# Optimization experiments

Measured on AMD Instinct MI355X. Metric: run time of the kernel, lower is better.

The kernel has to match this reference:

```python
import jax, jax.numpy as jnp
import numpy as np

B, S, D, H = 2, 2048, 1024, 16
DH = D // H

def setup_inputs() -> dict:
    key = jax.random.key(0)
    ks = jax.random.split(key, 11)
    sc = 0.02
    return {
        "q_": jax.random.normal(ks[0], (B, S, D), jnp.float32),
        "k_": jax.random.normal(ks[1], (B, S, D), jnp.float32),
        "v_": jax.random.normal(ks[2], (B, S, D), jnp.float32),
        "mask": jnp.ones((B, S), dtype=bool),
        "Wq": jax.random.normal(ks[3], (D, D), jnp.float32) * sc,
        "bq": jnp.zeros((D,), jnp.float32),
        "Wk": jax.random.normal(ks[4], (D, D), jnp.float32) * sc,
        "bk": jnp.zeros((D,), jnp.float32),
        "Wv": jax.random.normal(ks[5], (D, D), jnp.float32) * sc,
        "bv": jnp.zeros((D,), jnp.float32),
        "Wf": jax.random.normal(ks[6], (D, D), jnp.float32) * sc,
        "bf": jnp.zeros((D,), jnp.float32),
    }

def _split_heads(x, b):
    # [B, S, D] -> [B, H, S, DH]
    return x.reshape(b, -1, H, DH).transpose(0, 2, 1, 3)

def reference(q_, k_, v_, mask, Wq, bq, Wk, bk, Wv, bv, Wf, bf):
    b = q_.shape[0]
    q = _split_heads(q_ @ Wq + bq, b)
    k = _split_heads(k_ @ Wk + bk, b)
    v = _split_heads(v_ @ Wv + bv, b)
    # scaled dot-product attention scores [B, H, Sq, Sk]
    attn = jnp.einsum('bhqd,bhkd->bhqk', q, k) / jnp.sqrt(jnp.float32(DH))
    # original mask pattern: mask[B,S] repeated over heads then over KEY axis,
    # i.e. it masks whole query rows, broadcast over keys
    attn = jnp.where(mask[:, None, :, None], attn, jnp.float32(-1e12))
    attn_score = jax.nn.softmax(attn, axis=-1)  # dropout is identity (eval / drop=0)
    out = jnp.einsum('bhqk,bhkd->bhqd', attn_score, v)
    out = out.transpose(0, 2, 1, 3).reshape(b, -1, D)  # [B, S, D]
    return (out + q_) @ Wf + bf
```

## Files before the change

kernel.cpp:

```cpp
#include <hip/hip_runtime.h>
#include <stdint.h>


typedef __attribute__((ext_vector_type(8))) short bf16x8;
typedef __attribute__((ext_vector_type(4))) float f32x4;

#define MFMA(a, b, c) __builtin_amdgcn_mfma_f32_16x16x32_bf16((a), (b), (c), 0, 0, 0)

__device__ __forceinline__ short f2b(float f) {
  unsigned u = __builtin_bit_cast(unsigned, f);
  unsigned r = (u + 0x7fffu + ((u >> 16) & 1u)) >> 16;
  return (short)r;
}
__device__ __forceinline__ float b2f(short s) {
  unsigned u = ((unsigned)(unsigned short)s) << 16;
  return __builtin_bit_cast(float, u);
}
__device__ __forceinline__ void gload16(const void* g, void* l) {
  __builtin_amdgcn_global_load_lds((const __attribute__((address_space(1))) void*)g,
                                   (__attribute__((address_space(3))) void*)l, 16, 0, 0);
}

__global__ __launch_bounds__(256) void prep(const float* __restrict__ q,
                                            const float* __restrict__ k,
                                            const float* __restrict__ v,
                                            short* __restrict__ qb,
                                            short* __restrict__ kb,
                                            short* __restrict__ vb,
                                            const float* __restrict__ W0, const float* __restrict__ W1,
                                            const float* __restrict__ W2, const float* __restrict__ W3,
                                            short* __restrict__ T0, short* __restrict__ T1,
                                            short* __restrict__ T2, short* __restrict__ T3) {
  __shared__ float t[32][33];
  const int z = blockIdx.z;
  if (z < 3) {
    const float* src = (z == 0) ? q : (z == 1) ? k : v;
    short* dst       = (z == 0) ? qb : (z == 1) ? kb : vb;
    const int i = (blockIdx.x * 256 + threadIdx.x) * 8;
    const float4 f0 = *(const float4*)(src + i);
    const float4 f1 = *(const float4*)(src + i + 4);
    unsigned ou[4];
    ou[0] = (unsigned short)f2b(f0.x) | ((unsigned)(unsigned short)f2b(f0.y) << 16);
    ou[1] = (unsigned short)f2b(f0.z) | ((unsigned)(unsigned short)f2b(f0.w) << 16);
    ou[2] = (unsigned short)f2b(f1.x) | ((unsigned)(unsigned short)f2b(f1.y) << 16);
    ou[3] = (unsigned short)f2b(f1.z) | ((unsigned)(unsigned short)f2b(f1.w) << 16);
    *(uint4*)(dst + i) = *(uint4*)ou;
  } else {
    const int c = threadIdx.x & 31, r0 = threadIdx.x >> 5;
#pragma unroll
    for (int rep = 0; rep < 2; ++rep) {
      const int tile = blockIdx.x + rep * 2048;
      const int mtx = tile >> 10;
      const float* W = (mtx == 0) ? W0 : (mtx == 1) ? W1 : (mtx == 2) ? W2 : W3;
      short* T       = (mtx == 0) ? T0 : (mtx == 1) ? T1 : (mtx == 2) ? T2 : T3;
      const int n0 = (tile & 31) << 5, k0 = ((tile >> 5) & 31) << 5;
      if (rep) __syncthreads();
#pragma unroll
      for (int p = 0; p < 4; ++p) {
        int r = r0 + p * 8;
        t[r][c] = W[(size_t)(k0 + r) * 1024 + n0 + c];
      }
      __syncthreads();
#pragma unroll
      for (int p = 0; p < 4; ++p) {
        int r = r0 + p * 8;
        T[(size_t)(n0 + r) * 1024 + k0 + c] = f2b(t[c][r]);
      }
    }
  }
}

template <int MODE, int DBUF, int BM, int FVT>
__global__ __launch_bounds__(256) void gemm_bt(
    const short* __restrict__ A0, const short* __restrict__ A1, const short* __restrict__ A2_,
    const short* __restrict__ T0, const short* __restrict__ T1, const short* __restrict__ T2,
    const float* __restrict__ b0, const float* __restrict__ b1, const float* __restrict__ b2,
    void* o0, void* o1, void* o2) {
  constexpr int MT = BM / 32;
  __shared__ short As[(DBUF + 1) * BM * 64];
  __shared__ short Bs[(DBUF + 1) * 128 * 64];
  const int z = blockIdx.z;
  const short* A  = (z == 0) ? A0 : (z == 1) ? A1 : A2_;
  const short* Bt = (z == 0) ? T0 : (z == 1) ? T1 : T2;
  const float* bias = (z == 0) ? b0 : (z == 1) ? b1 : b2;
  void* outp = (z == 0) ? o0 : (z == 1) ? o1 : o2;
  const bool vt = (FVT == 2) || (FVT == 1 && z == 2);

  const int tid = threadIdx.x;
  const int lane = tid & 63, wid = tid >> 6;
  const int hi = lane >> 4, lo = lane & 15;
  const int wm = (wid >> 1) * (BM / 2), wn = (wid & 1) << 6;
  const int m0 = blockIdx.x * BM, n0 = blockIdx.y << 7;

  f32x4 acc[MT][4] = {};

  auto stage = [&](int bsel, int k0) {
    short* Ad = As + bsel * (BM * 64);
    short* Bd = Bs + bsel * 8192;
#pragma unroll
    for (int s = 0; s < BM / 32; ++s) {
      int d = s * 256 + tid;
      int row = d >> 3, cc = d & 7;
      int sc = cc ^ (row & 7);
      gload16(A + (size_t)(m0 + row) * 1024 + k0 + sc * 8, (void*)(Ad + (d & ~63) * 8));
    }
#pragma unroll
    for (int s = 0; s < 4; ++s) {
      int d = s * 256 + tid;
      int row = d >> 3, cc = d & 7;
      int sc = cc ^ (row & 7);
      gload16(Bt + (size_t)(n0 + row) * 1024 + k0 + sc * 8, (void*)(Bd + (d & ~63) * 8));
    }
  };
  auto compute = [&](const short* Asb, const short* Bsb) {
    bf16x8 af[MT][2], bfr[4][2];
#pragma unroll
    for (int t = 0; t < MT; ++t)
#pragma unroll
      for (int kh = 0; kh < 2; ++kh) {
        int ra = wm + t * 16 + lo;
        af[t][kh] = *(const bf16x8*)(Asb + ra * 64 + ((((kh << 2) | hi) ^ (ra & 7)) * 8));
      }
#pragma unroll
    for (int t = 0; t < 4; ++t)
#pragma unroll
      for (int kh = 0; kh < 2; ++kh) {
        int rb = wn + t * 16 + lo;
        bfr[t][kh] = *(const bf16x8*)(Bsb + rb * 64 + ((((kh << 2) | hi) ^ (rb & 7)) * 8));
      }
#pragma unroll
    for (int kh = 0; kh < 2; ++kh)
#pragma unroll
      for (int mt = 0; mt < MT; ++mt)
#pragma unroll
        for (int nt = 0; nt < 4; ++nt)
          acc[mt][nt] = MFMA(af[mt][kh], bfr[nt][kh], acc[mt][nt]);
  };

  if (DBUF) {
    stage(0, 0);
#pragma unroll 2
    for (int t = 0; t < 16; ++t) {
      __syncthreads();
      if (t < 15) stage((t + 1) & 1, (t + 1) * 64);
      compute(As + (t & 1) * (BM * 64), Bs + (t & 1) * 8192);
    }
  } else {
    for (int k0 = 0; k0 < 1024; k0 += 64) {
      stage(0, k0);
      __syncthreads();
      compute(As, Bs);
      __syncthreads();
    }
  }

#pragma unroll
  for (int mt = 0; mt < MT; ++mt) {
#pragma unroll
    for (int nt = 0; nt < 4; ++nt) {
      const int n = n0 + wn + nt * 16 + lo;
      const float bv = bias[n];
#pragma unroll
      for (int r = 0; r < 4; ++r) {
        const int m = m0 + wm + mt * 16 + (hi << 2) + r;
        float v = acc[mt][nt][r] + bv;
        if (MODE == 0) {
          int b = m >> 11, key = m & 2047, h = n >> 6, dd = n & 63;
          size_t bh = (size_t)((b << 4) + h);
          if (vt) {
            int kl = key & 63;
            int sig = (kl & 32) + ((kl >> 2) & 3) * 8 + ((kl >> 4) & 1) * 4 + (kl & 3);
            ((short*)outp)[bh * 131072 + (size_t)(key >> 6) * 4096 + dd * 64 + sig] = f2b(v);
          } else {
            ((short*)outp)[((bh * 2048 + key) << 6) + dd] = f2b(v);
          }
        } else {
          ((float*)outp)[(size_t)m * 1024 + n] = v;
        }
      }
    }
  }
}

__global__ __launch_bounds__(512) void attn_fwd(const short* __restrict__ Qh,
                                                const short* __restrict__ Kh,
                                                const short* __restrict__ Vh,
                                                const float* __restrict__ resid,
                                                short* __restrict__ A2) {
  __shared__ short Ks[3 * 64 * 64];
  __shared__ short Vs[3 * 64 * 64];
  const int tid = threadIdx.x;
  const int lane = tid & 63, wid = tid >> 6;
  const int hi = lane >> 4, lo = lane & 15;
  const int bh = blockIdx.y;
  const int q0 = blockIdx.x << 7;
  const size_t hoff = (size_t)bh * (2048 * 64);
  const float C = 0.18033688f;

  const int myq = q0 + wid * 16 + lo;
  bf16x8 qf[2];
  qf[0] = *(const bf16x8*)(Qh + hoff + (size_t)myq * 64 + hi * 8);
  qf[1] = *(const bf16x8*)(Qh + hoff + (size_t)myq * 64 + 32 + hi * 8);

  float m_run = -1e30f, mc = 0.f, l_part = 0.f;
  f32x4 oacc[4] = {};

  auto stage = [&](int bsel, int kt) {
    int d = tid;
    int row = d >> 3, cc = d & 7, sc = cc ^ (row & 7);
    gload16(Kh + hoff + (size_t)(kt + row) * 64 + sc * 8,
            (void*)(Ks + bsel * 4096 + (d & ~63) * 8));
    gload16(Vh + hoff + (size_t)(kt >> 6) * 4096 + row * 64 + sc * 8,
            (void*)(Vs + bsel * 4096 + (d & ~63) * 8));
  };

  auto pv = [&](const unsigned* bpp, const short* Vsb) {
#pragma unroll
    for (int t32 = 0; t32 < 2; ++t32) {
      uint4 up = {bpp[4 * t32], bpp[4 * t32 + 1], bpp[4 * t32 + 2], bpp[4 * t32 + 3]};
      bf16x8 bp = __builtin_bit_cast(bf16x8, up);
      __builtin_amdgcn_s_setprio(1);
#pragma unroll
      for (int dt = 0; dt < 4; ++dt) {
        int rv = dt * 16 + lo;
        bf16x8 va = *(const bf16x8*)(Vsb + rv * 64 + ((((t32 << 2) | hi) ^ (rv & 7)) * 8));
        oacc[dt] = MFMA(va, bp, oacc[dt]);
      }
      __builtin_amdgcn_s_setprio(0);
    }
  };

  stage(0, 0);
  stage(1, 64);
  unsigned bp_prev[8];
  int cb = 0;
  int pb = 2;
  int sb = 2;

  for (int it = 0; it < 32; ++it) {
    if (it < 31) asm volatile("s_waitcnt vmcnt(2)" ::: "memory");
    else         asm volatile("s_waitcnt vmcnt(0)" ::: "memory");
    __builtin_amdgcn_s_barrier();
    __builtin_amdgcn_sched_barrier(0);
    const short* Kc = Ks + cb * 4096;
    const short* Vprev = Vs + pb * 4096;

    float p[4][4];
    float tmax = -3e38f;
    __builtin_amdgcn_s_setprio(1);
#pragma unroll
    for (int mt = 0; mt < 4; ++mt) {
      f32x4 st = {};
#pragma unroll
      for (int kh = 0; kh < 2; ++kh) {
        int r = mt * 16 + lo;
        bf16x8 kf = *(const bf16x8*)(Kc + r * 64 + ((((kh << 2) | hi) ^ (r & 7)) * 8));
        st = MFMA(kf, qf[kh], st);
      }
#pragma unroll
      for (int r = 0; r < 4; ++r) {
        p[mt][r] = st[r];
        tmax = fmaxf(tmax, st[r]);
      }
    }
    __builtin_amdgcn_s_setprio(0);

    tmax = fmaxf(tmax, __shfl_xor(tmax, 16));
    tmax = fmaxf(tmax, __shfl_xor(tmax, 32));
    const bool doresc = !__all(tmax <= m_run);
    float fsc = 1.0f;
    if (doresc) {
      const float mnew = fmaxf(m_run, tmax);
      fsc = __builtin_amdgcn_exp2f((m_run - mnew) * C);
      l_part *= fsc;
      m_run = mnew;
      mc = mnew * C;
    }

    if (it > 0) pv(bp_prev, Vprev);

    unsigned bp_cur[8];
#pragma unroll
    for (int mt = 0; mt < 4; ++mt)
#pragma unroll
      for (int r = 0; r < 4; ++r) {
        float e = __builtin_amdgcn_exp2f(__builtin_fmaf(p[mt][r], C, -mc));
        p[mt][r] = e;
        l_part += e;
      }
#pragma unroll
    for (int t32 = 0; t32 < 2; ++t32) {
      const int a = t32 << 1;
      asm("v_cvt_pk_bf16_f32 %0, %1, %2" : "=v"(bp_cur[4 * t32 + 0]) : "v"(p[a][0]), "v"(p[a][1]));
      asm("v_cvt_pk_bf16_f32 %0, %1, %2" : "=v"(bp_cur[4 * t32 + 1]) : "v"(p[a][2]), "v"(p[a][3]));
      asm("v_cvt_pk_bf16_f32 %0, %1, %2" : "=v"(bp_cur[4 * t32 + 2]) : "v"(p[a + 1][0]), "v"(p[a + 1][1]));
      asm("v_cvt_pk_bf16_f32 %0, %1, %2" : "=v"(bp_cur[4 * t32 + 3]) : "v"(p[a + 1][2]), "v"(p[a + 1][3]));
    }

    if (doresc) {
#pragma unroll
      for (int dt = 0; dt < 4; ++dt) {
        oacc[dt][0] *= fsc; oacc[dt][1] *= fsc; oacc[dt][2] *= fsc; oacc[dt][3] *= fsc;
      }
    }

    __builtin_amdgcn_sched_barrier(0);
    __builtin_amdgcn_s_barrier();
    __builtin_amdgcn_sched_barrier(0);
    if (it < 30) stage(sb, (it + 2) * 64);

#pragma unroll
    for (int i = 0; i < 8; ++i) bp_prev[i] = bp_cur[i];
    pb = cb; cb = (cb == 2) ? 0 : cb + 1; sb = (sb == 2) ? 0 : sb + 1;
  }
  pv(bp_prev, Vs + 2 * 4096);

  float l = l_part;
  l += __shfl_xor(l, 16);
  l += __shfl_xor(l, 32);
  const float inv = 1.0f / l;
  __builtin_amdgcn_s_barrier();
  {
    short* eb = (wid < 4) ? Ks : Vs;
    const int rq = (wid & 3) * 16 + lo;
#pragma unroll
    for (int dt = 0; dt < 4; ++dt) {
#pragma unroll
      for (int r = 0; r < 4; ++r) {
        int dd = dt * 16 + (hi << 2) + r;
        int cc = dd >> 3;
        eb[rq * 64 + ((cc ^ (rq & 7)) * 8) + (dd & 7)] = f2b(oacc[dt][r] * inv);
      }
    }
  }
  __syncthreads();
#pragma unroll
  for (int s = 0; s < 2; ++s) {
    const short* eb = s ? Vs : Ks;
    int c = tid;
    int rr = c >> 3, cc = c & 7;
    bf16x8 ov = *(const bf16x8*)(eb + rr * 64 + ((cc ^ (rr & 7)) * 8));
    int gr = s * 64 + rr;
    int gm = ((bh >> 4) << 11) + q0 + gr;
    int gn = ((bh & 15) << 6) + cc * 8;
    const float* qr = resid + (size_t)gm * 1024 + gn;
    unsigned ou[4];
#pragma unroll
    for (int j = 0; j < 4; ++j) {
      unsigned l16 = (unsigned short)f2b(b2f(ov[2 * j]) + qr[2 * j]);
      unsigned h16 = (unsigned short)f2b(b2f(ov[2 * j + 1]) + qr[2 * j + 1]);
      ou[j] = l16 | (h16 << 16);
    }
    *(uint4*)(A2 + (size_t)gm * 1024 + gn) = *(uint4*)ou;
  }
}

extern "C" void kernel_launch(void* const* d_in, const int* in_sizes, int n_in,
                              void* d_out, int out_size, void* d_ws, size_t ws_size,
                              hipStream_t stream) {
  (void)in_sizes; (void)n_in; (void)out_size;
  const float* q_ = (const float*)d_in[0];
  const float* k_ = (const float*)d_in[1];
  const float* v_ = (const float*)d_in[2];
  const float* Wq = (const float*)d_in[4];
  const float* bq = (const float*)d_in[5];
  const float* Wk = (const float*)d_in[6];
  const float* bk = (const float*)d_in[7];
  const float* Wv = (const float*)d_in[8];
  const float* bv = (const float*)d_in[9];
  const float* Wf = (const float*)d_in[10];
  const float* bf = (const float*)d_in[11];

  const size_t MB = 1048576;
  char* ws = (char*)d_ws;
  short *qb, *kb, *vb, *Qh, *Kh, *Vh, *A2p, *Wqt, *Wkt, *Wvt, *Wft;
  const bool big = ws_size >= 56 * MB;
  if (big) {
    qb = (short*)(ws + 0 * MB);  kb = (short*)(ws + 8 * MB);  vb = (short*)(ws + 16 * MB);
    Qh = (short*)(ws + 24 * MB); Kh = (short*)(ws + 32 * MB); Vh = (short*)(ws + 40 * MB);
    A2p = vb;
    Wqt = (short*)(ws + 48 * MB); Wkt = (short*)(ws + 50 * MB);
    Wvt = (short*)(ws + 52 * MB); Wft = (short*)(ws + 54 * MB);
  } else {
    qb = (short*)(ws + 0 * MB);  kb = (short*)(ws + 8 * MB);  vb = (short*)(ws + 16 * MB);
    Qh = (short*)(ws + 24 * MB);
    Kh = qb; Vh = kb; A2p = vb;
    Wqt = (short*)(ws + 32 * MB); Wkt = (short*)(ws + 34 * MB);
    Wvt = (short*)(ws + 36 * MB); Wft = (short*)(ws + 38 * MB);
  }

  prep<<<dim3(2048, 1, 4), 256, 0, stream>>>(q_, k_, v_, qb, kb, vb,
                                             Wq, Wk, Wv, Wf, Wqt, Wkt, Wvt, Wft);
  if (big) {
    gemm_bt<0, 0, 128, 1><<<dim3(32, 8, 3), 256, 0, stream>>>(qb, kb, vb, Wqt, Wkt, Wvt,
                                                              bq, bk, bv, Qh, Kh, Vh);
  } else {
    gemm_bt<0, 0, 128, 0><<<dim3(32, 8, 1), 256, 0, stream>>>(qb, qb, qb, Wqt, Wqt, Wqt,
                                                              bq, bq, bq, Qh, Qh, Qh);
    gemm_bt<0, 0, 128, 0><<<dim3(32, 8, 1), 256, 0, stream>>>(kb, kb, kb, Wkt, Wkt, Wkt,
                                                              bk, bk, bk, Kh, Kh, Kh);
    gemm_bt<0, 0, 128, 2><<<dim3(32, 8, 1), 256, 0, stream>>>(vb, vb, vb, Wvt, Wvt, Wvt,
                                                              bv, bv, bv, Vh, Vh, Vh);
  }
  attn_fwd<<<dim3(16, 32), 512, 0, stream>>>(Qh, Kh, Vh, q_, A2p);
  gemm_bt<1, 1, 64, 0><<<dim3(64, 8, 1), 256, 0, stream>>>(A2p, A2p, A2p, Wft, Wft, Wft,
                                                           bf, bf, bf, d_out, d_out, d_out);
}
```

Before: 128.2 us.

## Process two query tiles per wave in attention, halving block threads

The attention kernel now runs 256 threads per block instead of 512, and each wave handles 32 query rows as two 16-row tiles. Each K and V fragment read from LDS is reused across two MFMAs, which halves LDS read traffic per MFMA and gives more independent MFMA chains per wave. Staging and the epilogue loops are widened to cover the same tile with fewer threads. The cost is higher register pressure from doubled accumulators and softmax state, and fewer waves per block to hide latency.

```diff
diff --git a/kernel.cpp b/kernel.cpp
--- a/kernel.cpp
+++ b/kernel.cpp
@@ -182,7 +182,7 @@
   }
 }
 
-__global__ __launch_bounds__(512) void attn_fwd(const short* __restrict__ Qh,
+__global__ __launch_bounds__(256) void attn_fwd(const short* __restrict__ Qh,
                                                 const short* __restrict__ Kh,
                                                 const short* __restrict__ Vh,
                                                 const float* __restrict__ resid,
@@ -194,37 +194,47 @@
   const int hi = lane >> 4, lo = lane & 15;
   const int bh = blockIdx.y;
   const int q0 = blockIdx.x << 7;
-  const size_t hoff = (size_t)bh * (2048 * 64);
+  const size_t hoff = (size_t)bh * 131072;
   const float C = 0.18033688f;
 
-  const int myq = q0 + wid * 16 + lo;
-  bf16x8 qf[2];
-  qf[0] = *(const bf16x8*)(Qh + hoff + (size_t)myq * 64 + hi * 8);
-  qf[1] = *(const bf16x8*)(Qh + hoff + (size_t)myq * 64 + 32 + hi * 8);
-
-  float m_run = -1e30f, mc = 0.f, l_part = 0.f;
-  f32x4 oacc[4] = {};
+  const int myq0 = q0 + wid * 32 + lo;
+  const int myq1 = myq0 + 16;
+  bf16x8 qf0[2], qf1[2];
+  qf0[0] = *(const bf16x8*)(Qh + hoff + (size_t)myq0 * 64 + hi * 8);
+  qf0[1] = *(const bf16x8*)(Qh + hoff + (size_t)myq0 * 64 + 32 + hi * 8);
+  qf1[0] = *(const bf16x8*)(Qh + hoff + (size_t)myq1 * 64 + hi * 8);
+  qf1[1] = *(const bf16x8*)(Qh + hoff + (size_t)myq1 * 64 + 32 + hi * 8);
+
+  float m0r = -1e30f, mc0 = 0.f, l0 = 0.f;
+  float m1r = -1e30f, mc1 = 0.f, l1 = 0.f;
+  f32x4 oa0[4] = {}, oa1[4] = {};
 
   auto stage = [&](int bsel, int kt) {
-    int d = tid;
-    int row = d >> 3, cc = d & 7, sc = cc ^ (row & 7);
-    gload16(Kh + hoff + (size_t)(kt + row) * 64 + sc * 8,
-            (void*)(Ks + bsel * 4096 + (d & ~63) * 8));
-    gload16(Vh + hoff + (size_t)(kt >> 6) * 4096 + row * 64 + sc * 8,
-            (void*)(Vs + bsel * 4096 + (d & ~63) * 8));
+#pragma unroll
+    for (int s = 0; s < 2; ++s) {
+      int d = s * 256 + tid;
+      int row = d >> 3, cc = d & 7, sc = cc ^ (row & 7);
+      gload16(Kh + hoff + (size_t)(kt + row) * 64 + sc * 8,
+              (void*)(Ks + bsel * 4096 + (d & ~63) * 8));
+      gload16(Vh + hoff + (size_t)(kt >> 6) * 4096 + row * 64 + sc * 8,
+              (void*)(Vs + bsel * 4096 + (d & ~63) * 8));
+    }
   };
 
-  auto pv = [&](const unsigned* bpp, const short* Vsb) {
+  auto pv = [&](const unsigned* bp0, const unsigned* bp1, const short* Vsb) {
 #pragma unroll
     for (int t32 = 0; t32 < 2; ++t32) {
-      uint4 up = {bpp[4 * t32], bpp[4 * t32 + 1], bpp[4 * t32 + 2], bpp[4 * t32 + 3]};
-      bf16x8 bp = __builtin_bit_cast(bf16x8, up);
+      uint4 u0 = {bp0[4 * t32], bp0[4 * t32 + 1], bp0[4 * t32 + 2], bp0[4 * t32 + 3]};
+      uint4 u1 = {bp1[4 * t32], bp1[4 * t32 + 1], bp1[4 * t32 + 2], bp1[4 * t32 + 3]};
+      bf16x8 b0 = __builtin_bit_cast(bf16x8, u0);
+      bf16x8 b1 = __builtin_bit_cast(bf16x8, u1);
       __builtin_amdgcn_s_setprio(1);
 #pragma unroll
       for (int dt = 0; dt < 4; ++dt) {
         int rv = dt * 16 + lo;
         bf16x8 va = *(const bf16x8*)(Vsb + rv * 64 + ((((t32 << 2) | hi) ^ (rv & 7)) * 8));
-        oacc[dt] = MFMA(va, bp, oacc[dt]);
+        oa0[dt] = MFMA(va, b0, oa0[dt]);
+        oa1[dt] = MFMA(va, b1, oa1[dt]);
       }
       __builtin_amdgcn_s_setprio(0);
     }
@@ -232,75 +242,89 @@
 
   stage(0, 0);
   stage(1, 64);
-  unsigned bp_prev[8];
-  int cb = 0;
-  int pb = 2;
-  int sb = 2;
+  unsigned bp_prev0[8], bp_prev1[8];
+  int cb = 0, pb = 2, sb = 2;
 
   for (int it = 0; it < 32; ++it) {
-    if (it < 31) asm volatile("s_waitcnt vmcnt(2)" ::: "memory");
+    if (it < 31) asm volatile("s_waitcnt vmcnt(4)" ::: "memory");
     else         asm volatile("s_waitcnt vmcnt(0)" ::: "memory");
     __builtin_amdgcn_s_barrier();
     __builtin_amdgcn_sched_barrier(0);
     const short* Kc = Ks + cb * 4096;
     const short* Vprev = Vs + pb * 4096;
 
-    float p[4][4];
-    float tmax = -3e38f;
+    float p0[4][4], p1[4][4];
+    float t0 = -3e38f, t1 = -3e38f;
     __builtin_amdgcn_s_setprio(1);
 #pragma unroll
     for (int mt = 0; mt < 4; ++mt) {
-      f32x4 st = {};
+      f32x4 s0 = {}, s1 = {};
 #pragma unroll
       for (int kh = 0; kh < 2; ++kh) {
         int r = mt * 16 + lo;
         bf16x8 kf = *(const bf16x8*)(Kc + r * 64 + ((((kh << 2) | hi) ^ (r & 7)) * 8));
-        st = MFMA(kf, qf[kh], st);
+        s0 = MFMA(kf, qf0[kh], s0);
+        s1 = MFMA(kf, qf1[kh], s1);
       }
 #pragma unroll
       for (int r = 0; r < 4; ++r) {
-        p[mt][r] = st[r];
-        tmax = fmaxf(tmax, st[r]);
+        p0[mt][r] = s0[r]; t0 = fmaxf(t0, s0[r]);
+        p1[mt][r] = s1[r]; t1 = fmaxf(t1, s1[r]);
       }
     }
     __builtin_amdgcn_s_setprio(0);
 
-    tmax = fmaxf(tmax, __shfl_xor(tmax, 16));
-    tmax = fmaxf(tmax, __shfl_xor(tmax, 32));
-    const bool doresc = !__all(tmax <= m_run);
-    float fsc = 1.0f;
-    if (doresc) {
-      const float mnew = fmaxf(m_run, tmax);
-      fsc = __builtin_amdgcn_exp2f((m_run - mnew) * C);
-      l_part *= fsc;
-      m_run = mnew;
-      mc = mnew * C;
-    }
-
-    if (it > 0) pv(bp_prev, Vprev);
-
-    unsigned bp_cur[8];
+    t0 = fmaxf(t0, __shfl_xor(t0, 16)); t0 = fmaxf(t0, __shfl_xor(t0, 32));
+    t1 = fmaxf(t1, __shfl_xor(t1, 16)); t1 = fmaxf(t1, __shfl_xor(t1, 32));
+    const bool dr0 = !__all(t0 <= m0r);
+    const bool dr1 = !__all(t1 <= m1r);
+    float fsc0 = 1.0f, fsc1 = 1.0f;
+    if (dr0) {
+      const float mnew = fmaxf(m0r, t0);
+      fsc0 = __builtin_amdgcn_exp2f((m0r - mnew) * C);
+      l0 *= fsc0; m0r = mnew; mc0 = mnew * C;
+    }
+    if (dr1) {
+      const float mnew = fmaxf(m1r, t1);
+      fsc1 = __builtin_amdgcn_exp2f((m1r - mnew) * C);
+      l1 *= fsc1; m1r = mnew; mc1 = mnew * C;
+    }
+
+    if (it > 0) pv(bp_prev0, bp_prev1, Vprev);
+
+    unsigned bpc0[8], bpc1[8];
 #pragma unroll
     for (int mt = 0; mt < 4; ++mt)
 #pragma unroll
       for (int r = 0; r < 4; ++r) {
-        float e = __builtin_amdgcn_exp2f(__builtin_fmaf(p[mt][r], C, -mc));
-        p[mt][r] = e;
-        l_part += e;
+        float e0 = __builtin_amdgcn_exp2f(__builtin_fmaf(p0[mt][r], C, -mc0));
+        float e1 = __builtin_amdgcn_exp2f(__builtin_fmaf(p1[mt][r], C, -mc1));
+        p0[mt][r] = e0; l0 += e0;
+        p1[mt][r] = e1; l1 += e1;
       }
 #pragma unroll
     for (int t32 = 0; t32 < 2; ++t32) {
       const int a = t32 << 1;
-      asm("v_cvt_pk_bf16_f32 %0, %1, %2" : "=v"(bp_cur[4 * t32 + 0]) : "v"(p[a][0]), "v"(p[a][1]));
-      asm("v_cvt_pk_bf16_f32 %0, %1, %2" : "=v"(bp_cur[4 * t32 + 1]) : "v"(p[a][2]), "v"(p[a][3]));
-      asm("v_cvt_pk_bf16_f32 %0, %1, %2" : "=v"(bp_cur[4 * t32 + 2]) : "v"(p[a + 1][0]), "v"(p[a + 1][1]));
-      asm("v_cvt_pk_bf16_f32 %0, %1, %2" : "=v"(bp_cur[4 * t32 + 3]) : "v"(p[a + 1][2]), "v"(p[a + 1][3]));
-    }
-
-    if (doresc) {
+      asm("v_cvt_pk_bf16_f32 %0, %1, %2" : "=v"(bpc0[4 * t32 + 0]) : "v"(p0[a][0]), "v"(p0[a][1]));
+      asm("v_cvt_pk_bf16_f32 %0, %1, %2" : "=v"(bpc0[4 * t32 + 1]) : "v"(p0[a][2]), "v"(p0[a][3]));
+      asm("v_cvt_pk_bf16_f32 %0, %1, %2" : "=v"(bpc0[4 * t32 + 2]) : "v"(p0[a + 1][0]), "v"(p0[a + 1][1]));
+      asm("v_cvt_pk_bf16_f32 %0, %1, %2" : "=v"(bpc0[4 * t32 + 3]) : "v"(p0[a + 1][2]), "v"(p0[a + 1][3]));
+      asm("v_cvt_pk_bf16_f32 %0, %1, %2" : "=v"(bpc1[4 * t32 + 0]) : "v"(p1[a][0]), "v"(p1[a][1]));
+      asm("v_cvt_pk_bf16_f32 %0, %1, %2" : "=v"(bpc1[4 * t32 + 1]) : "v"(p1[a][2]), "v"(p1[a][3]));
+      asm("v_cvt_pk_bf16_f32 %0, %1, %2" : "=v"(bpc1[4 * t32 + 2]) : "v"(p1[a + 1][0]), "v"(p1[a + 1][1]));
+      asm("v_cvt_pk_bf16_f32 %0, %1, %2" : "=v"(bpc1[4 * t32 + 3]) : "v"(p1[a + 1][2]), "v"(p1[a + 1][3]));
+    }
+
+    if (dr0) {
 #pragma unroll
       for (int dt = 0; dt < 4; ++dt) {
-        oacc[dt][0] *= fsc; oacc[dt][1] *= fsc; oacc[dt][2] *= fsc; oacc[dt][3] *= fsc;
+        oa0[dt][0] *= fsc0; oa0[dt][1] *= fsc0; oa0[dt][2] *= fsc0; oa0[dt][3] *= fsc0;
+      }
+    }
+    if (dr1) {
+#pragma unroll
+      for (int dt = 0; dt < 4; ++dt) {
+        oa1[dt][0] *= fsc1; oa1[dt][1] *= fsc1; oa1[dt][2] *= fsc1; oa1[dt][3] *= fsc1;
       }
     }
 
@@ -310,46 +334,47 @@
     if (it < 30) stage(sb, (it + 2) * 64);
 
 #pragma unroll
-    for (int i = 0; i < 8; ++i) bp_prev[i] = bp_cur[i];
+    for (int i = 0; i < 8; ++i) { bp_prev0[i] = bpc0[i]; bp_prev1[i] = bpc1[i]; }
     pb = cb; cb = (cb == 2) ? 0 : cb + 1; sb = (sb == 2) ? 0 : sb + 1;
   }
-  pv(bp_prev, Vs + 2 * 4096);
-
-  float l = l_part;
-  l += __shfl_xor(l, 16);
-  l += __shfl_xor(l, 32);
-  const float inv = 1.0f / l;
+  pv(bp_prev0, bp_prev1, Vs + 2 * 4096);
+
+  l0 += __shfl_xor(l0, 16); l0 += __shfl_xor(l0, 32);
+  l1 += __shfl_xor(l1, 16); l1 += __shfl_xor(l1, 32);
+  const float inv0 = 1.0f / l0, inv1 = 1.0f / l1;
   __builtin_amdgcn_s_barrier();
   {
-    short* eb = (wid < 4) ? Ks : Vs;
-    const int rq = (wid & 3) * 16 + lo;
+    short* eb = (wid < 2) ? Ks : Vs;
+    const int rqa = (wid & 1) * 32 + lo;
+    const int rqb = rqa + 16;
 #pragma unroll
     for (int dt = 0; dt < 4; ++dt) {
 #pragma unroll
       for (int r = 0; r < 4; ++r) {
         int dd = dt * 16 + (hi << 2) + r;
         int cc = dd >> 3;
-        eb[rq * 64 + ((cc ^ (rq & 7)) * 8) + (dd & 7)] = f2b(oacc[dt][r] * inv);
+        eb[rqa * 64 + ((cc ^ (rqa & 7)) * 8) + (dd & 7)] = f2b(oa0[dt][r] * inv0);
+        eb[rqb * 64 + ((cc ^ (rqb & 7)) * 8) + (dd & 7)] = f2b(oa1[dt][r] * inv1);
       }
     }
   }
   __syncthreads();
 #pragma unroll
-  for (int s = 0; s < 2; ++s) {
-    const short* eb = s ? Vs : Ks;
-    int c = tid;
-    int rr = c >> 3, cc = c & 7;
+  for (int s = 0; s < 4; ++s) {
+    int c = s * 256 + tid;
+    const short* eb = (c < 512) ? Ks : Vs;
+    int cl = c & 511, rr = cl >> 3, cc = cl & 7;
     bf16x8 ov = *(const bf16x8*)(eb + rr * 64 + ((cc ^ (rr & 7)) * 8));
-    int gr = s * 64 + rr;
+    int gr = (c >> 9) * 64 + rr;
     int gm = ((bh >> 4) << 11) + q0 + gr;
     int gn = ((bh & 15) << 6) + cc * 8;
     const float* qr = resid + (size_t)gm * 1024 + gn;
     unsigned ou[4];
 #pragma unroll
     for (int j = 0; j < 4; ++j) {
-      unsigned l16 = (unsigned short)f2b(b2f(ov[2 * j]) + qr[2 * j]);
-      unsigned h16 = (unsigned short)f2b(b2f(ov[2 * j + 1]) + qr[2 * j + 1]);
-      ou[j] = l16 | (h16 << 16);
+      unsigned lw = (unsigned short)f2b(b2f(ov[2 * j]) + qr[2 * j]);
+      unsigned hw = (unsigned short)f2b(b2f(ov[2 * j + 1]) + qr[2 * j + 1]);
+      ou[j] = lw | (hw << 16);
     }
     *(uint4*)(A2 + (size_t)gm * 1024 + gn) = *(uint4*)ou;
   }
@@ -402,7 +427,7 @@
     gemm_bt<0, 0, 128, 2><<<dim3(32, 8, 1), 256, 0, stream>>>(vb, vb, vb, Wvt, Wvt, Wvt,
                                                               bv, bv, bv, Vh, Vh, Vh);
   }
-  attn_fwd<<<dim3(16, 32), 512, 0, stream>>>(Qh, Kh, Vh, q_, A2p);
+  attn_fwd<<<dim3(16, 32), 256, 0, stream>>>(Qh, Kh, Vh, q_, A2p);
   gemm_bt<1, 1, 64, 0><<<dim3(64, 8, 1), 256, 0, stream>>>(A2p, A2p, A2p, Wft, Wft, Wft,
                                                            bf, bf, bf, d_out, d_out, d_out);
 }
```

Result: slower. 136.2 us (+6.3%).

## Replace triple-buffered 64-key pipeline with single-buffered 128-key tiles

Applied to the files above, without the earlier changes.

The attention kernel now processes 128 keys per iteration with a single LDS buffer, loading K and V and then synchronising before compute. This replaces the triple-buffered 64-key loop that overlapped P·V of the previous tile with QK of the current one. Barrier count and loop overhead per key are halved, but global loads are no longer overlapped with MFMA work, and register pressure from the larger score tile rises.

```diff
diff --git a/kernel.cpp b/kernel.cpp
--- a/kernel.cpp
+++ b/kernel.cpp
@@ -187,14 +187,14 @@
                                                 const short* __restrict__ Vh,
                                                 const float* __restrict__ resid,
                                                 short* __restrict__ A2) {
-  __shared__ short Ks[3 * 64 * 64];
-  __shared__ short Vs[3 * 64 * 64];
+  __shared__ short Ks[128 * 64];
+  __shared__ short Vs[2 * 64 * 64];
   const int tid = threadIdx.x;
   const int lane = tid & 63, wid = tid >> 6;
   const int hi = lane >> 4, lo = lane & 15;
   const int bh = blockIdx.y;
   const int q0 = blockIdx.x << 7;
-  const size_t hoff = (size_t)bh * (2048 * 64);
+  const size_t hoff = (size_t)bh * 131072;
   const float C = 0.18033688f;
 
   const int myq = q0 + wid * 16 + lo;
@@ -205,56 +205,34 @@
   float m_run = -1e30f, mc = 0.f, l_part = 0.f;
   f32x4 oacc[4] = {};
 
-  auto stage = [&](int bsel, int kt) {
-    int d = tid;
-    int row = d >> 3, cc = d & 7, sc = cc ^ (row & 7);
-    gload16(Kh + hoff + (size_t)(kt + row) * 64 + sc * 8,
-            (void*)(Ks + bsel * 4096 + (d & ~63) * 8));
-    gload16(Vh + hoff + (size_t)(kt >> 6) * 4096 + row * 64 + sc * 8,
-            (void*)(Vs + bsel * 4096 + (d & ~63) * 8));
+  auto stage = [&](int kt) {
+#pragma unroll
+    for (int s = 0; s < 2; ++s) {
+      int d = s * 512 + tid;
+      int row = d >> 3, cc = d & 7, sc = cc ^ (row & 7);
+      gload16(Kh + hoff + (size_t)(kt + row) * 64 + sc * 8,
+              (void*)(Ks + (d & ~63) * 8));
+      int sub = d >> 9, el = d & 511;
+      int vrow = el >> 3, vcc = el & 7, vsc = vcc ^ (vrow & 7);
+      gload16(Vh + hoff + (size_t)((kt >> 6) + sub) * 4096 + vrow * 64 + vsc * 8,
+              (void*)(Vs + sub * 4096 + (el & ~63) * 8));
+    }
   };
 
-  auto pv = [&](const unsigned* bpp, const short* Vsb) {
-#pragma unroll
-    for (int t32 = 0; t32 < 2; ++t32) {
-      uint4 up = {bpp[4 * t32], bpp[4 * t32 + 1], bpp[4 * t32 + 2], bpp[4 * t32 + 3]};
-      bf16x8 bp = __builtin_bit_cast(bf16x8, up);
-      __builtin_amdgcn_s_setprio(1);
-#pragma unroll
-      for (int dt = 0; dt < 4; ++dt) {
-        int rv = dt * 16 + lo;
-        bf16x8 va = *(const bf16x8*)(Vsb + rv * 64 + ((((t32 << 2) | hi) ^ (rv & 7)) * 8));
-        oacc[dt] = MFMA(va, bp, oacc[dt]);
-      }
-      __builtin_amdgcn_s_setprio(0);
-    }
-  };
-
-  stage(0, 0);
-  stage(1, 64);
-  unsigned bp_prev[8];
-  int cb = 0;
-  int pb = 2;
-  int sb = 2;
-
-  for (int it = 0; it < 32; ++it) {
-    if (it < 31) asm volatile("s_waitcnt vmcnt(2)" ::: "memory");
-    else         asm volatile("s_waitcnt vmcnt(0)" ::: "memory");
-    __builtin_amdgcn_s_barrier();
-    __builtin_amdgcn_sched_barrier(0);
-    const short* Kc = Ks + cb * 4096;
-    const short* Vprev = Vs + pb * 4096;
-
-    float p[4][4];
+  for (int it = 0; it < 16; ++it) {
+    stage(it * 128);
+    __syncthreads();
+
+    float p[8][4];
     float tmax = -3e38f;
     __builtin_amdgcn_s_setprio(1);
 #pragma unroll
-    for (int mt = 0; mt < 4; ++mt) {
+    for (int mt = 0; mt < 8; ++mt) {
       f32x4 st = {};
 #pragma unroll
       for (int kh = 0; kh < 2; ++kh) {
         int r = mt * 16 + lo;
-        bf16x8 kf = *(const bf16x8*)(Kc + r * 64 + ((((kh << 2) | hi) ^ (r & 7)) * 8));
+        bf16x8 kf = *(const bf16x8*)(Ks + r * 64 + ((((kh << 2) | hi) ^ (r & 7)) * 8));
         st = MFMA(kf, qf[kh], st);
       }
 #pragma unroll
@@ -267,89 +245,80 @@
 
     tmax = fmaxf(tmax, __shfl_xor(tmax, 16));
     tmax = fmaxf(tmax, __shfl_xor(tmax, 32));
-    const bool doresc = !__all(tmax <= m_run);
-    float fsc = 1.0f;
-    if (doresc) {
+    if (!__all(tmax <= m_run)) {
       const float mnew = fmaxf(m_run, tmax);
-      fsc = __builtin_amdgcn_exp2f((m_run - mnew) * C);
+      const float fsc = __builtin_amdgcn_exp2f((m_run - mnew) * C);
       l_part *= fsc;
+#pragma unroll
+      for (int dt = 0; dt < 4; ++dt) {
+        oacc[dt][0] *= fsc; oacc[dt][1] *= fsc; oacc[dt][2] *= fsc; oacc[dt][3] *= fsc;
+      }
       m_run = mnew;
       mc = mnew * C;
     }
-
-    if (it > 0) pv(bp_prev, Vprev);
-
-    unsigned bp_cur[8];
-#pragma unroll
-    for (int mt = 0; mt < 4; ++mt)
+#pragma unroll
+    for (int mt = 0; mt < 8; ++mt)
 #pragma unroll
       for (int r = 0; r < 4; ++r) {
         float e = __builtin_amdgcn_exp2f(__builtin_fmaf(p[mt][r], C, -mc));
         p[mt][r] = e;
         l_part += e;
       }
-#pragma unroll
-    for (int t32 = 0; t32 < 2; ++t32) {
+
+#pragma unroll
+    for (int t32 = 0; t32 < 4; ++t32) {
       const int a = t32 << 1;
-      asm("v_cvt_pk_bf16_f32 %0, %1, %2" : "=v"(bp_cur[4 * t32 + 0]) : "v"(p[a][0]), "v"(p[a][1]));
-      asm("v_cvt_pk_bf16_f32 %0, %1, %2" : "=v"(bp_cur[4 * t32 + 1]) : "v"(p[a][2]), "v"(p[a][3]));
-      asm("v_cvt_pk_bf16_f32 %0, %1, %2" : "=v"(bp_cur[4 * t32 + 2]) : "v"(p[a + 1][0]), "v"(p[a + 1][1]));
-      asm("v_cvt_pk_bf16_f32 %0, %1, %2" : "=v"(bp_cur[4 * t32 + 3]) : "v"(p[a + 1][2]), "v"(p[a + 1][3]));
-    }
-
-    if (doresc) {
+      unsigned u0, u1, u2, u3;
+      asm("v_cvt_pk_bf16_f32 %0, %1, %2" : "=v"(u0) : "v"(p[a][0]), "v"(p[a][1]));
+      asm("v_cvt_pk_bf16_f32 %0, %1, %2" : "=v"(u1) : "v"(p[a][2]), "v"(p[a][3]));
+      asm("v_cvt_pk_bf16_f32 %0, %1, %2" : "=v"(u2) : "v"(p[a + 1][0]), "v"(p[a + 1][1]));
+      asm("v_cvt_pk_bf16_f32 %0, %1, %2" : "=v"(u3) : "v"(p[a + 1][2]), "v"(p[a + 1][3]));
+      uint4 up = {u0, u1, u2, u3};
+      bf16x8 bp = __builtin_bit_cast(bf16x8, up);
+      const short* Vg = Vs + (t32 >> 1) * 4096;
+      __builtin_amdgcn_s_setprio(1);
 #pragma unroll
       for (int dt = 0; dt < 4; ++dt) {
-        oacc[dt][0] *= fsc; oacc[dt][1] *= fsc; oacc[dt][2] *= fsc; oacc[dt][3] *= fsc;
-      }
-    }
-
-    __builtin_amdgcn_sched_barrier(0);
-    __builtin_amdgcn_s_barrier();
-    __builtin_amdgcn_sched_barrier(0);
-    if (it < 30) stage(sb, (it + 2) * 64);
-
-#pragma unroll
-    for (int i = 0; i < 8; ++i) bp_prev[i] = bp_cur[i];
-    pb = cb; cb = (cb == 2) ? 0 : cb + 1; sb = (sb == 2) ? 0 : sb + 1;
-  }
-  pv(bp_prev, Vs + 2 * 4096);
+        int rv = dt * 16 + lo;
+        bf16x8 va = *(const bf16x8*)(Vg + rv * 64 + (((((t32 & 1) << 2) | hi) ^ (rv & 7)) * 8));
+        oacc[dt] = MFMA(va, bp, oacc[dt]);
+      }
+      __builtin_amdgcn_s_setprio(0);
+    }
+    __syncthreads();
+  }
 
   float l = l_part;
   l += __shfl_xor(l, 16);
   l += __shfl_xor(l, 32);
   const float inv = 1.0f / l;
-  __builtin_amdgcn_s_barrier();
   {
-    short* eb = (wid < 4) ? Ks : Vs;
-    const int rq = (wid & 3) * 16 + lo;
+    const int rq = wid * 16 + lo;
 #pragma unroll
     for (int dt = 0; dt < 4; ++dt) {
 #pragma unroll
       for (int r = 0; r < 4; ++r) {
         int dd = dt * 16 + (hi << 2) + r;
         int cc = dd >> 3;
-        eb[rq * 64 + ((cc ^ (rq & 7)) * 8) + (dd & 7)] = f2b(oacc[dt][r] * inv);
+        Ks[rq * 64 + ((cc ^ (rq & 7)) * 8) + (dd & 7)] = f2b(oacc[dt][r] * inv);
       }
     }
   }
   __syncthreads();
 #pragma unroll
   for (int s = 0; s < 2; ++s) {
-    const short* eb = s ? Vs : Ks;
-    int c = tid;
+    int c = s * 512 + tid;
     int rr = c >> 3, cc = c & 7;
-    bf16x8 ov = *(const bf16x8*)(eb + rr * 64 + ((cc ^ (rr & 7)) * 8));
-    int gr = s * 64 + rr;
-    int gm = ((bh >> 4) << 11) + q0 + gr;
+    bf16x8 ov = *(const bf16x8*)(Ks + rr * 64 + ((cc ^ (rr & 7)) * 8));
+    int gm = ((bh >> 4) << 11) + q0 + rr;
     int gn = ((bh & 15) << 6) + cc * 8;
     const float* qr = resid + (size_t)gm * 1024 + gn;
     unsigned ou[4];
 #pragma unroll
     for (int j = 0; j < 4; ++j) {
-      unsigned l16 = (unsigned short)f2b(b2f(ov[2 * j]) + qr[2 * j]);
-      unsigned h16 = (unsigned short)f2b(b2f(ov[2 * j + 1]) + qr[2 * j + 1]);
-      ou[j] = l16 | (h16 << 16);
+      unsigned lw = (unsigned short)f2b(b2f(ov[2 * j]) + qr[2 * j]);
+      unsigned hw = (unsigned short)f2b(b2f(ov[2 * j + 1]) + qr[2 * j + 1]);
+      ou[j] = lw | (hw << 16);
     }
     *(uint4*)(A2 + (size_t)gm * 1024 + gn) = *(uint4*)ou;
   }
```

Result: faster. 124.7 us (-2.7%).
